# Kernel optimization log

Measured on AMD Instinct MI355X. Metric: run time of the kernel, lower is better.

Reference implementation:

```python
import jax, jax.numpy as jnp
import numpy as np
from jax import lax

B, S, T = 32, 128, 64          # batch, src_len, trg_len
E, H = 64, 512                 # embed_dim, hidden_size
SRC_V, TRG_V = 32000, 32000


def gru_cell(x, h, W_ih, W_hh, b_ih, b_hh):
    """PyTorch-convention GRU cell. x:[B,I], h:[B,H] -> h':[B,H]"""
    gi = x @ W_ih.T + b_ih            # [B,3H]
    gh = h @ W_hh.T + b_hh            # [B,3H]
    i_r, i_z, i_n = jnp.split(gi, 3, axis=-1)
    h_r, h_z, h_n = jnp.split(gh, 3, axis=-1)
    r = jax.nn.sigmoid(i_r + h_r)
    z = jax.nn.sigmoid(i_z + h_z)
    n = jnp.tanh(i_n + r * h_n)
    return (1.0 - z) * n + z * h


def setup_inputs() -> dict:
    key = jax.random.key(0)
    ks = jax.random.split(key, 22)
    g = lambda i, shape: jax.random.normal(ks[i], shape, jnp.float32) * 0.05
    return {
        "src": jax.random.randint(ks[0], (B, S), 0, SRC_V),
        "trg": jax.random.randint(ks[1], (B, T), 0, TRG_V),
        "src_embed": g(2, (SRC_V, E)),
        "trg_embed": g(3, (TRG_V, E)),
        # encoder GRU (1 layer, input E)
        "enc_W_ih": g(4, (3 * H, E)), "enc_W_hh": g(5, (3 * H, H)),
        "enc_b_ih": g(6, (3 * H,)), "enc_b_hh": g(7, (3 * H,)),
        # decoder GRU layer 0 (input E+H due to attention concat)
        "dec0_W_ih": g(8, (3 * H, E + H)), "dec0_W_hh": g(9, (3 * H, H)),
        "dec0_b_ih": g(10, (3 * H,)), "dec0_b_hh": g(11, (3 * H,)),
        # decoder GRU layer 1 (input H)
        "dec1_W_ih": g(12, (3 * H, H)), "dec1_W_hh": g(13, (3 * H, H)),
        "dec1_b_ih": g(14, (3 * H,)), "dec1_b_hh": g(15, (3 * H,)),
        # additive attention: energy = tanh(W[h;enc]) , score = v^T energy
        "attn_W": g(16, (H, 2 * H)), "attn_b": g(17, (H,)),
        "v_W": g(18, (1, H)), "v_b": jnp.zeros((1,), jnp.float32),
        # output projection H -> TRG_V
        "fc_W": g(19, (TRG_V, H)), "fc_b": jnp.zeros((TRG_V,), jnp.float32),
    }


def reference(src, trg, src_embed, trg_embed,
              enc_W_ih, enc_W_hh, enc_b_ih, enc_b_hh,
              dec0_W_ih, dec0_W_hh, dec0_b_ih, dec0_b_hh,
              dec1_W_ih, dec1_W_hh, dec1_b_ih, dec1_b_hh,
              attn_W, attn_b, v_W, v_b, fc_W, fc_b):
    batch = src.shape[0]
    src_e = src_embed[src]                              # [B,S,E]

    # ---- encoder: 1-layer GRU over src ----
    def enc_step(h, x):
        h2 = gru_cell(x, h, enc_W_ih, enc_W_hh, enc_b_ih, enc_b_hh)
        return h2, h2
    h0 = jnp.zeros((batch, H), src_e.dtype)
    h_last, enc_outs = lax.scan(enc_step, h0, jnp.swapaxes(src_e, 0, 1))
    enc_outs = jnp.swapaxes(enc_outs, 0, 1)             # [B,S,H]

    # _adapt_hidden: replicate last encoder layer to 2 decoder layers
    carry0 = (h_last, h_last)

    # ---- decoder: teacher forcing (ratio=1.0), steps t=1..T-1 ----
    def dec_step(carry, tok):
        h0_, h1_ = carry
        # attention context from top decoder layer hidden
        q = jnp.concatenate(
            [jnp.broadcast_to(h1_[:, None, :], enc_outs.shape), enc_outs], axis=-1)  # [B,S,2H]
        energy = jnp.tanh(q @ attn_W.T + attn_b)        # [B,S,H]
        scores = energy @ v_W[0] + v_b[0]               # [B,S]
        w = jax.nn.softmax(scores, axis=-1)
        context = jnp.einsum('bs,bsh->bh', w, enc_outs) # [B,H]
        emb = jnp.concatenate([trg_embed[tok], context], axis=-1)  # [B,E+H]
        h0n = gru_cell(emb, h0_, dec0_W_ih, dec0_W_hh, dec0_b_ih, dec0_b_hh)
        h1n = gru_cell(h0n, h1_, dec1_W_ih, dec1_W_hh, dec1_b_ih, dec1_b_hh)
        logits = h1n @ fc_W.T + fc_b                    # [B,V]
        return (h0n, h1n), logits

    tokens = jnp.swapaxes(trg[:, :-1], 0, 1)            # inputs for t=1..T-1
    _, logits = lax.scan(dec_step, carry0, tokens)      # [T-1,B,V]
    outputs = jnp.concatenate(
        [jnp.zeros((batch, 1, TRG_V), logits.dtype), jnp.swapaxes(logits, 0, 1)], axis=1)
    return outputs                                       # [B,T,V]
```

## Files before the change

kernel.cpp:

```cpp
#include <hip/hip_runtime.h>
#include <hip/hip_bf16.h>

#define BB 32
#define SS 128
#define TT 64
#define EE 64
#define HH 512
#define H3 1536
#define VV 32000
#define EHD 576
#define TD 63
#define MFC 2048

typedef unsigned short u16;
typedef unsigned int   u32;

typedef __attribute__((ext_vector_type(8))) short bf16x8;
typedef __attribute__((ext_vector_type(4))) float f32x4;

__device__ __forceinline__ float bf2f(u16 u){ return __uint_as_float(((u32)u)<<16); }
__device__ __forceinline__ u16 f2bf(float f){
  u32 u = __float_as_uint(f);
  u += 0x7FFFu + ((u>>16)&1u);
  return (u16)(u>>16);
}
__device__ __forceinline__ float sigm(float x){ return 1.f/(1.f+__expf(-x)); }
__device__ __forceinline__ float tanh_f(float x){ return 1.f - 2.f/(1.f+__expf(2.f*x)); }

__device__ __forceinline__ void bf8f(uint4 q, float* f){
  f[0]=__uint_as_float(q.x<<16); f[1]=__uint_as_float(q.x&0xFFFF0000u);
  f[2]=__uint_as_float(q.y<<16); f[3]=__uint_as_float(q.y&0xFFFF0000u);
  f[4]=__uint_as_float(q.z<<16); f[5]=__uint_as_float(q.z&0xFFFF0000u);
  f[6]=__uint_as_float(q.w<<16); f[7]=__uint_as_float(q.w&0xFFFF0000u);
}

template<bool BF>
__device__ __forceinline__ void wload8(const void* base, size_t eoff, float* f){
  if constexpr (BF){
    uint4 q = *(const uint4*)((const u16*)base + eoff);
    bf8f(q, f);
  } else {
    const float4* p = (const float4*)((const float*)base + eoff);
    float4 a = p[0], b = p[1];
    f[0]=a.x; f[1]=a.y; f[2]=a.z; f[3]=a.w;
    f[4]=b.x; f[5]=b.y; f[6]=b.z; f[7]=b.w;
  }
}
template<bool BF>
__device__ __forceinline__ float wld(const void* base, size_t eoff){
  if constexpr (BF) return bf2f(((const u16*)base)[eoff]);
  else              return ((const float*)base)[eoff];
}
template<bool BF>
__device__ __forceinline__ void stage32(const void* gbase, size_t eoff, u16* lds){
  if constexpr (BF){
    const uint4* g = (const uint4*)((const u16*)gbase + eoff);
    uint4* l = (uint4*)lds;
    l[0]=g[0]; l[1]=g[1]; l[2]=g[2]; l[3]=g[3];
  } else {
    const float4* g = (const float4*)((const float*)gbase + eoff);
    #pragma unroll
    for(int i=0;i<8;i++){
      float4 v = g[i];
      u16* d = lds + i*4;
      d[0]=f2bf(v.x); d[1]=f2bf(v.y); d[2]=f2bf(v.z); d[3]=f2bf(v.w);
    }
  }
}

__global__ __launch_bounds__(64) void k_detect(const void* w, int* flag){
  int tid = threadIdx.x;
  const u16* p = (const u16*)w;
  float m = 0.f;
  #pragma unroll
  for(int i=0;i<16;i++){
    float v = fabsf(bf2f(p[tid*16+i]));
    m = fmaxf(m, v);
  }
  #pragma unroll
  for(int off=32;off;off>>=1) m = fmaxf(m, __shfl_down(m, off));
  if(tid==0) *flag = (m < 16.f) ? 1 : 0;
}

template<bool BF>
__device__ void emb_gi_body(const int* toks, int tstride, const void* emb_tab,
                            const void* W_ih, int wstride, const void* b_ih,
                            float* gi)
{
  int blk = blockIdx.x;
  int jc = blk % 6; int b = (blk/6) % BB; int t = blk/(6*BB);
  int tid = threadIdx.x;
  int tok = toks[b*tstride + t];
  __shared__ float emb[EE];
  if(tid < EE) emb[tid] = wld<BF>(emb_tab, (size_t)tok*EE + tid);
  __syncthreads();
  int j = jc*256 + tid;
  float acc = wld<BF>(b_ih, j);
  size_t roff = (size_t)j*wstride;
  #pragma unroll
  for(int i=0;i<8;i++){
    float f[8]; wload8<BF>(W_ih, roff + i*8, f);
    #pragma unroll
    for(int l=0;l<8;l++) acc += emb[i*8+l]*f[l];
  }
  gi[((size_t)t*BB + b)*H3 + j] = acc;
}
__global__ __launch_bounds__(256) void k_emb_gi(
    const int* flag, const int* toks, int tstride, const void* emb_tab,
    const void* W_ih, int wstride, const void* b_ih, float* gi)
{
  if(*flag) emb_gi_body<true>(toks,tstride,emb_tab,W_ih,wstride,b_ih,gi);
  else      emb_gi_body<false>(toks,tstride,emb_tab,W_ih,wstride,b_ih,gi);
}

template<bool BF>
__device__ void enc_step_body(const float* hin, float* hout,
                              const void* W_hh, const void* b_hh,
                              const float* gi_t, float* enc_outs, int t,
                              float* h0init, float* h1init)
{
  int b = blockIdx.x >> 3, q = blockIdx.x & 7;
  int tid = threadIdx.x;
  __shared__ float hs[HH];
  __shared__ float red[3][256];
  const float* hrow = hin + b*HH;
  hs[tid] = hrow[tid]; hs[tid+256] = hrow[tid+256];
  __syncthreads();
  int jj = tid >> 2, t4 = tid & 3;
  int j = q*64 + jj;
  int k0 = t4*128;
  float ar=0.f, az=0.f, an=0.f;
  size_t orr = (size_t)j*HH + k0;
  size_t oz = (size_t)(512+j)*HH + k0;
  size_t on = (size_t)(1024+j)*HH + k0;
  #pragma unroll 4
  for(int i=0;i<16;i++){
    float f[8];
    wload8<BF>(W_hh, orr + i*8, f);
    #pragma unroll
    for(int l=0;l<8;l++) ar += hs[k0+i*8+l]*f[l];
    wload8<BF>(W_hh, oz + i*8, f);
    #pragma unroll
    for(int l=0;l<8;l++) az += hs[k0+i*8+l]*f[l];
    wload8<BF>(W_hh, on + i*8, f);
    #pragma unroll
    for(int l=0;l<8;l++) an += hs[k0+i*8+l]*f[l];
  }
  red[0][tid]=ar; red[1][tid]=az; red[2][tid]=an;
  __syncthreads();
  if(t4==0){
    float gr = red[0][tid]+red[0][tid+1]+red[0][tid+2]+red[0][tid+3] + wld<BF>(b_hh, j);
    float gz = red[1][tid]+red[1][tid+1]+red[1][tid+2]+red[1][tid+3] + wld<BF>(b_hh, 512+j);
    float gn = red[2][tid]+red[2][tid+1]+red[2][tid+2]+red[2][tid+3] + wld<BF>(b_hh, 1024+j);
    const float* gib = gi_t + b*H3;
    float r = sigm(gib[j] + gr);
    float z = sigm(gib[512+j] + gz);
    float n = tanh_f(gib[1024+j] + r*gn);
    float hn = (1.f - z)*n + z*hs[j];
    hout[b*HH + j] = hn;
    enc_outs[((size_t)b*SS + t)*HH + j] = hn;
    if(h0init){ h0init[b*HH+j] = hn; h1init[b*HH+j] = hn; }
  }
}
__global__ __launch_bounds__(256) void k_enc_step(
    const int* flag, const float* hin, float* hout,
    const void* W_hh, const void* b_hh, const float* gi_t,
    float* enc_outs, int t, float* h0init, float* h1init)
{
  if(*flag) enc_step_body<true>(hin,hout,W_hh,b_hh,gi_t,enc_outs,t,h0init,h1init);
  else      enc_step_body<false>(hin,hout,W_hh,b_hh,gi_t,enc_outs,t,h0init,h1init);
}

template<bool BF>
__device__ void attn_proj_body(const float* enc_outs, const void* attn_W,
                               const void* attn_b, float* P)
{
  int blk = blockIdx.x;
  int jc = blk & 1; int s = (blk>>1) & (SS-1); int b = blk >> 8;
  int tid = threadIdx.x;
  __shared__ float es[HH];
  const float* er = enc_outs + ((size_t)b*SS + s)*HH;
  es[tid]=er[tid]; es[tid+256]=er[tid+256];
  __syncthreads();
  int j = jc*256 + tid;
  size_t roff = (size_t)j*1024 + 512;
  float acc = wld<BF>(attn_b, j);
  #pragma unroll 4
  for(int i=0;i<64;i++){
    float f[8]; wload8<BF>(attn_W, roff + i*8, f);
    #pragma unroll
    for(int l=0;l<8;l++) acc += es[i*8+l]*f[l];
  }
  P[((size_t)b*SS+s)*HH + j] = acc;
}
__global__ __launch_bounds__(256) void k_attn_proj(
  const int* flag, const float* enc_outs, const void* attn_W,
  const void* attn_b, float* P)
{
  if(*flag) attn_proj_body<true>(enc_outs, attn_W, attn_b, P);
  else      attn_proj_body<false>(enc_outs, attn_W, attn_b, P);
}

template<bool BF>
__device__ void dec_A_body(const float* h1, const void* attn_W, float* Abuf)
{
  int b = blockIdx.x >> 1, jc = blockIdx.x & 1;
  int tid = threadIdx.x;
  __shared__ float hsr[HH];
  hsr[tid]=h1[b*HH+tid]; hsr[tid+256]=h1[b*HH+tid+256];
  __syncthreads();
  int j = jc*256 + tid;
  size_t roff = (size_t)j*1024;
  float acc = 0.f;
  #pragma unroll 4
  for(int i=0;i<64;i++){
    float f[8]; wload8<BF>(attn_W, roff + i*8, f);
    #pragma unroll
    for(int l=0;l<8;l++) acc += hsr[i*8+l]*f[l];
  }
  Abuf[b*HH + j] = acc;
}
__global__ __launch_bounds__(256) void k_dec_A(
  const int* flag, const float* h1, const void* attn_W, float* Abuf)
{
  if(*flag) dec_A_body<true>(h1, attn_W, Abuf);
  else      dec_A_body<false>(h1, attn_W, Abuf);
}

template<bool BF>
__device__ void dec_scores_body(const float* Abuf, const float* P,
                                const float* enc_outs, const void* vW,
                                const void* vb, float* Cpart, float* Ssum)
{
  int b = blockIdx.x >> 3, sb = blockIdx.x & 7;
  int tid = threadIdx.x;
  __shared__ float As[HH];
  __shared__ float vs[HH];
  __shared__ float eS[16];
  As[tid]=Abuf[b*HH+tid]; As[tid+256]=Abuf[b*HH+tid+256];
  vs[tid]=wld<BF>(vW, tid); vs[tid+256]=wld<BF>(vW, tid+256);
  __syncthreads();
  int wave = tid>>6, lane = tid&63;
  float vbf = wld<BF>(vb, 0);
  #pragma unroll
  for(int i=0;i<4;i++){
    int s = sb*16 + wave*4 + i;
    const float* Prow = P + ((size_t)b*SS+s)*HH;
    float part = 0.f;
    #pragma unroll
    for(int kk=0;kk<8;kk++){
      int k = lane + kk*64;
      part += vs[k]*tanh_f(As[k]+Prow[k]);
    }
    #pragma unroll
    for(int off=32;off;off>>=1) part += __shfl_down(part, off);
    if(lane==0) eS[wave*4+i] = __expf(part + vbf);
  }
  __syncthreads();
  for(int j=tid;j<HH;j+=256){
    float c = 0.f;
    #pragma unroll 4
    for(int i=0;i<16;i++) c += eS[i]*enc_outs[((size_t)b*SS + sb*16+i)*HH + j];
    Cpart[((size_t)b*8+sb)*HH + j] = c;
  }
  if(tid==0){ float ss=0.f; for(int i=0;i<16;i++) ss+=eS[i]; Ssum[b*8+sb]=ss; }
}
__global__ __launch_bounds__(256) void k_dec_scores(
  const int* flag, const float* Abuf, const float* P, const float* enc_outs,
  const void* vW, const void* vb, float* Cpart, float* Ssum)
{
  if(*flag) dec_scores_body<true>(Abuf,P,enc_outs,vW,vb,Cpart,Ssum);
  else      dec_scores_body<false>(Abuf,P,enc_outs,vW,vb,Cpart,Ssum);
}

template<bool BF>
__device__ void dec_h0_body(const float* h0in, float* h0out,
                            const float* Cpart, const float* Ssum,
                            const void* W_ih, const void* W_hh,
                            const void* b_hh, const float* gi_t)
{
  int b = blockIdx.x >> 3, q = blockIdx.x & 7;
  int tid = threadIdx.x;
  __shared__ float ctx[HH];
  __shared__ float hs[HH];
  __shared__ float red[6][256];
  const float* hr = h0in + b*HH;
  hs[tid]=hr[tid]; hs[tid+256]=hr[tid+256];
  float ssum = 0.f;
  #pragma unroll
  for(int sb=0;sb<8;sb++) ssum += Ssum[b*8+sb];
  float invS = 1.f/ssum;
  for(int j=tid;j<HH;j+=256){
    float c = 0.f;
    #pragma unroll
    for(int sb=0;sb<8;sb++) c += Cpart[((size_t)b*8+sb)*HH + j];
    ctx[j] = c*invS;
  }
  __syncthreads();
  int jj = tid>>2, t4 = tid&3, j = q*64+jj, k0 = t4*128;
  float pr=0.f,pz=0.f,pn=0.f,qr=0.f,qz=0.f,qn=0.f;
  size_t oir = (size_t)j*EHD + 64 + k0;
  size_t oiz = (size_t)(512+j)*EHD + 64 + k0;
  size_t oin = (size_t)(1024+j)*EHD + 64 + k0;
  size_t ohr = (size_t)j*HH + k0;
  size_t ohz = (size_t)(512+j)*HH + k0;
  size_t ohn = (size_t)(1024+j)*HH + k0;
  #pragma unroll 2
  for(int i=0;i<16;i++){
    float f[8];
    wload8<BF>(W_ih, oir + i*8, f);
    #pragma unroll
    for(int l=0;l<8;l++) pr += ctx[k0+i*8+l]*f[l];
    wload8<BF>(W_ih, oiz + i*8, f);
    #pragma unroll
    for(int l=0;l<8;l++) pz += ctx[k0+i*8+l]*f[l];
    wload8<BF>(W_ih, oin + i*8, f);
    #pragma unroll
    for(int l=0;l<8;l++) pn += ctx[k0+i*8+l]*f[l];
    wload8<BF>(W_hh, ohr + i*8, f);
    #pragma unroll
    for(int l=0;l<8;l++) qr += hs[k0+i*8+l]*f[l];
    wload8<BF>(W_hh, ohz + i*8, f);
    #pragma unroll
    for(int l=0;l<8;l++) qz += hs[k0+i*8+l]*f[l];
    wload8<BF>(W_hh, ohn + i*8, f);
    #pragma unroll
    for(int l=0;l<8;l++) qn += hs[k0+i*8+l]*f[l];
  }
  red[0][tid]=pr; red[1][tid]=pz; red[2][tid]=pn;
  red[3][tid]=qr; red[4][tid]=qz; red[5][tid]=qn;
  __syncthreads();
  if(t4==0){
    float gir = gi_t[b*H3 + j]        + red[0][tid]+red[0][tid+1]+red[0][tid+2]+red[0][tid+3];
    float giz = gi_t[b*H3 + 512 + j]  + red[1][tid]+red[1][tid+1]+red[1][tid+2]+red[1][tid+3];
    float gin = gi_t[b*H3 + 1024 + j] + red[2][tid]+red[2][tid+1]+red[2][tid+2]+red[2][tid+3];
    float ghr = red[3][tid]+red[3][tid+1]+red[3][tid+2]+red[3][tid+3] + wld<BF>(b_hh, j);
    float ghz = red[4][tid]+red[4][tid+1]+red[4][tid+2]+red[4][tid+3] + wld<BF>(b_hh, 512+j);
    float ghn = red[5][tid]+red[5][tid+1]+red[5][tid+2]+red[5][tid+3] + wld<BF>(b_hh, 1024+j);
    float r = sigm(gir+ghr), z = sigm(giz+ghz), n = tanh_f(gin + r*ghn);
    h0out[b*HH + j] = (1.f - z)*n + z*hs[j];
  }
}
__global__ __launch_bounds__(256) void k_dec_h0(
  const int* flag, const float* h0in, float* h0out,
  const float* Cpart, const float* Ssum,
  const void* W_ih, const void* W_hh, const void* b_hh, const float* gi_t)
{
  if(*flag) dec_h0_body<true>(h0in,h0out,Cpart,Ssum,W_ih,W_hh,b_hh,gi_t);
  else      dec_h0_body<false>(h0in,h0out,Cpart,Ssum,W_ih,W_hh,b_hh,gi_t);
}

template<bool BF>
__device__ void dec_h1_body(const float* xin, const float* h1in, float* h1out,
                            const void* W_ih, const void* b_ih,
                            const void* W_hh, const void* b_hh,
                            u16* h1_all_t)
{
  int b = blockIdx.x >> 3, q = blockIdx.x & 7;
  int tid = threadIdx.x;
  __shared__ float xs[HH];
  __shared__ float hs[HH];
  __shared__ float red[6][256];
  const float* xr = xin + b*HH;
  const float* hr = h1in + b*HH;
  xs[tid]=xr[tid]; xs[tid+256]=xr[tid+256];
  hs[tid]=hr[tid]; hs[tid+256]=hr[tid+256];
  __syncthreads();
  int jj = tid>>2, t4 = tid&3, j = q*64+jj, k0 = t4*128;
  float pr=0.f,pz=0.f,pn=0.f,qr=0.f,qz=0.f,qn=0.f;
  size_t oir = (size_t)j*HH + k0;
  size_t oiz = (size_t)(512+j)*HH + k0;
  size_t oin = (size_t)(1024+j)*HH + k0;
  #pragma unroll 2
  for(int i=0;i<16;i++){
    float f[8];
    wload8<BF>(W_ih, oir + i*8, f);
    #pragma unroll
    for(int l=0;l<8;l++) pr += xs[k0+i*8+l]*f[l];
    wload8<BF>(W_ih, oiz + i*8, f);
    #pragma unroll
    for(int l=0;l<8;l++) pz += xs[k0+i*8+l]*f[l];
    wload8<BF>(W_ih, oin + i*8, f);
    #pragma unroll
    for(int l=0;l<8;l++) pn += xs[k0+i*8+l]*f[l];
    wload8<BF>(W_hh, oir + i*8, f);
    #pragma unroll
    for(int l=0;l<8;l++) qr += hs[k0+i*8+l]*f[l];
    wload8<BF>(W_hh, oiz + i*8, f);
    #pragma unroll
    for(int l=0;l<8;l++) qz += hs[k0+i*8+l]*f[l];
    wload8<BF>(W_hh, oin + i*8, f);
    #pragma unroll
    for(int l=0;l<8;l++) qn += hs[k0+i*8+l]*f[l];
  }
  red[0][tid]=pr; red[1][tid]=pz; red[2][tid]=pn;
  red[3][tid]=qr; red[4][tid]=qz; red[5][tid]=qn;
  __syncthreads();
  if(t4==0){
    float gir = wld<BF>(b_ih, j)      + red[0][tid]+red[0][tid+1]+red[0][tid+2]+red[0][tid+3];
    float giz = wld<BF>(b_ih, 512+j)  + red[1][tid]+red[1][tid+1]+red[1][tid+2]+red[1][tid+3];
    float gin = wld<BF>(b_ih, 1024+j) + red[2][tid]+red[2][tid+1]+red[2][tid+2]+red[2][tid+3];
    float ghr = red[3][tid]+red[3][tid+1]+red[3][tid+2]+red[3][tid+3] + wld<BF>(b_hh, j);
    float ghz = red[4][tid]+red[4][tid+1]+red[4][tid+2]+red[4][tid+3] + wld<BF>(b_hh, 512+j);
    float ghn = red[5][tid]+red[5][tid+1]+red[5][tid+2]+red[5][tid+3] + wld<BF>(b_hh, 1024+j);
    float r = sigm(gir+ghr), z = sigm(giz+ghz), n = tanh_f(gin + r*ghn);
    float hn = (1.f - z)*n + z*hs[j];
    h1out[b*HH + j] = hn;
    h1_all_t[b*HH + j] = f2bf(hn);
  }
}
__global__ __launch_bounds__(256) void k_dec_h1(
  const int* flag, const float* xin, const float* h1in, float* h1out,
  const void* W_ih, const void* b_ih, const void* W_hh, const void* b_hh,
  u16* h1_all_t)
{
  if(*flag) dec_h1_body<true>(xin,h1in,h1out,W_ih,b_ih,W_hh,b_hh,h1_all_t);
  else      dec_h1_body<false>(xin,h1in,h1out,W_ih,b_ih,W_hh,b_hh,h1_all_t);
}

__global__ __launch_bounds__(256) void k_zero_t0(const int* flag, void* out){
  int idx = blockIdx.x*256 + threadIdx.x;
  int b = idx / VV, v = idx - b*VV;
  size_t o = (size_t)b*TT*VV + v;
  if(*flag) ((u16*)out)[o] = 0;
  else      ((float*)out)[o] = 0.f;
}

template<bool BF>
__device__ void fc_body(const u16* A, const void* W, const void* bias, void* out)
{
  __shared__ u16 As[128*72];
  __shared__ u16 Bs[128*72];
  int bm = blockIdx.x, bn = blockIdx.y;
  int tid = threadIdx.x;
  int wave = tid>>6, lane = tid&63;
  int wr = wave>>1, wc = wave&1;
  f32x4 acc[4][4];
  f32x4 zero = {0.f,0.f,0.f,0.f};
  #pragma unroll
  for(int i=0;i<4;i++)
    #pragma unroll
    for(int j=0;j<4;j++) acc[i][j]=zero;

  int row = tid>>1, half = tid&1;
  const size_t gA = (size_t)(bm*128 + row)*512 + half*32;
  const size_t gB = (size_t)(bn*128 + row)*512 + half*32;
  u16* lA = As + row*72 + half*32;
  u16* lB = Bs + row*72 + half*32;

  for(int kk=0;kk<8;kk++){
    int k0 = kk*64;
    if(kk) __syncthreads();
    stage32<true>(A, gA + k0, lA);
    stage32<BF>(W, gB + k0, lB);
    __syncthreads();
    #pragma unroll
    for(int ks=0;ks<2;ks++){
      int kof = ks*32 + (lane>>4)*8;
      bf16x8 af[4], bfv[4];
      #pragma unroll
      for(int i=0;i<4;i++){
        af[i]  = *(const bf16x8*)(As + (wr*64 + i*16 + (lane&15))*72 + kof);
        bfv[i] = *(const bf16x8*)(Bs + (wc*64 + i*16 + (lane&15))*72 + kof);
      }
      #pragma unroll
      for(int i=0;i<4;i++)
        #pragma unroll
        for(int j=0;j<4;j++)
          acc[i][j] = __builtin_amdgcn_mfma_f32_16x16x32_bf16(af[i], bfv[j], acc[i][j], 0, 0, 0);
    }
  }
  int quad = lane>>4, col = lane&15;
  #pragma unroll
  for(int j=0;j<4;j++){
    int n = bn*128 + wc*64 + j*16 + col;
    float bsv = wld<BF>(bias, n);
    #pragma unroll
    for(int i=0;i<4;i++){
      int mbase = bm*128 + wr*64 + i*16 + quad*4;
      #pragma unroll
      for(int r=0;r<4;r++){
        int m = mbase + r;
        if(m < TD*BB){
          int t = m >> 5, b = m & 31;
          size_t o = ((size_t)(b*TT + t + 1))*VV + n;
          float v = acc[i][j][r] + bsv;
          if constexpr (BF) ((u16*)out)[o] = f2bf(v);
          else              ((float*)out)[o] = v;
        }
      }
    }
  }
}
__global__ __launch_bounds__(256) void k_fc(
  const int* flag, const u16* A, const void* W, const void* bias, void* out)
{
  if(*flag) fc_body<true>(A, W, bias, out);
  else      fc_body<false>(A, W, bias, out);
}

extern "C" void kernel_launch(void* const* d_in, const int* in_sizes, int n_in,
                              void* d_out, int out_size, void* d_ws, size_t ws_size,
                              hipStream_t stream)
{
  const int* src = (const int*)d_in[0];
  const int* trg = (const int*)d_in[1];
  const void* src_emb = d_in[2];
  const void* trg_emb = d_in[3];
  const void* eWih = d_in[4];
  const void* eWhh = d_in[5];
  const void* ebih = d_in[6];
  const void* ebhh = d_in[7];
  const void* d0Wih = d_in[8];
  const void* d0Whh = d_in[9];
  const void* d0bih = d_in[10];
  const void* d0bhh = d_in[11];
  const void* d1Wih = d_in[12];
  const void* d1Whh = d_in[13];
  const void* d1bih = d_in[14];
  const void* d1bhh = d_in[15];
  const void* aW  = d_in[16];
  const void* ab  = d_in[17];
  const void* vW  = d_in[18];
  const void* vb  = d_in[19];
  const void* fcW = d_in[20];
  const void* fcb = d_in[21];

  char* w = (char*)d_ws;
  int*   flag    = (int*)w;   w += 16;
  float* enc_gi  = (float*)w; w += (size_t)SS*BB*H3*4;
  float* trg_gi  = (float*)w; w += (size_t)TD*BB*H3*4;
  float* enc_outs= (float*)w; w += (size_t)BB*SS*HH*4;
  float* P       = (float*)w; w += (size_t)BB*SS*HH*4;
  float* hE      = (float*)w; w += (size_t)2*BB*HH*4;
  float* h0b     = (float*)w; w += (size_t)2*BB*HH*4;
  float* h1b     = (float*)w; w += (size_t)2*BB*HH*4;
  float* Abuf    = (float*)w; w += (size_t)BB*HH*4;
  float* Cpart   = (float*)w; w += (size_t)BB*8*HH*4;
  float* Ssum    = (float*)w; w += (size_t)BB*8*4;
  u16*   h1_all  = (u16*)w;   w += (size_t)MFC*HH*2;

  hipMemsetAsync(hE, 0, BB*HH*4, stream);
  hipMemsetAsync(h1_all + (size_t)TD*BB*HH, 0, 32*HH*2, stream);

  k_detect<<<1,64,0,stream>>>(fcW, flag);

  k_emb_gi<<<SS*BB*6, 256, 0, stream>>>(flag, src, SS, src_emb, eWih, EE, ebih, enc_gi);
  k_emb_gi<<<TD*BB*6, 256, 0, stream>>>(flag, trg, TT, trg_emb, d0Wih, EHD, d0bih, trg_gi);

  for(int t=0;t<SS;t++){
    k_enc_step<<<256,256,0,stream>>>(
      flag, hE + (t&1)*BB*HH, hE + ((t+1)&1)*BB*HH,
      eWhh, ebhh, enc_gi + (size_t)t*BB*H3, enc_outs, t,
      (t==SS-1)?h0b:(float*)nullptr, (t==SS-1)?h1b:(float*)nullptr);
  }

  k_attn_proj<<<BB*SS*2,256,0,stream>>>(flag, enc_outs, aW, ab, P);

  for(int t=0;t<TD;t++){
    int pi = t&1, po = (t+1)&1;
    k_dec_A<<<64,256,0,stream>>>(flag, h1b + pi*BB*HH, aW, Abuf);
    k_dec_scores<<<256,256,0,stream>>>(flag, Abuf, P, enc_outs, vW, vb, Cpart, Ssum);
    k_dec_h0<<<256,256,0,stream>>>(flag, h0b+pi*BB*HH, h0b+po*BB*HH, Cpart, Ssum,
                                   d0Wih, d0Whh, d0bhh, trg_gi + (size_t)t*BB*H3);
    k_dec_h1<<<256,256,0,stream>>>(flag, h0b+po*BB*HH, h1b+pi*BB*HH, h1b+po*BB*HH,
                                   d1Wih, d1bih, d1Whh, d1bhh, h1_all + (size_t)t*BB*HH);
  }

  k_zero_t0<<<(BB*VV)/256, 256, 0, stream>>>(flag, d_out);
  dim3 g(16, 250);
  k_fc<<<g, 256, 0, stream>>>(flag, h1_all, fcW, fcb, d_out);
}
```

Before: 7.828 ms.

## Fuse encoder/decoder recurrence into one persistent cooperative kernel with grid syncs

Replaces the hundreds of per-timestep kernel launches (encoder steps, attention projection, and four decoder stages per step) with a single cooperative kernel of 256 blocks that loops over time and uses grid-wide syncs between stages. Shared memory is unified into one struct reused across stages, and dec_A is re-partitioned to split the K dimension across 4 threads per output so it fits the 256-block layout. This removes launch overhead and inter-kernel gaps on the serial recurrence. In exchange, every stage pays for a grid barrier, and the attention projection becomes a serial loop of 32 iterations per block.

```diff
diff --git a/kernel.cpp b/kernel.cpp
--- a/kernel.cpp
+++ b/kernel.cpp
@@ -1,5 +1,8 @@
 #include <hip/hip_runtime.h>
 #include <hip/hip_bf16.h>
+#include <hip/hip_cooperative_groups.h>
+
+namespace cg = cooperative_groups;
 
 #define BB 32
 #define SS 128
@@ -113,16 +116,40 @@
   else      emb_gi_body<false>(toks,tstride,emb_tab,W_ih,wstride,b_ih,gi);
 }
 
-template<bool BF>
-__device__ void enc_step_body(const float* hin, float* hout,
-                              const void* W_hh, const void* b_hh,
-                              const float* gi_t, float* enc_outs, int t,
-                              float* h0init, float* h1init)
-{
-  int b = blockIdx.x >> 3, q = blockIdx.x & 7;
-  int tid = threadIdx.x;
-  __shared__ float hs[HH];
-  __shared__ float red[3][256];
+struct SMem {
+  float a[HH];
+  float b[HH];
+  float red[6][256];
+  float eS[16];
+};
+
+struct EncDecParams {
+  const int* flag;
+  const void *eWhh, *ebhh;
+  const float* enc_gi;
+  float* enc_outs;
+  const void *aW, *ab, *vW, *vb;
+  const void *d0Wih, *d0Whh, *d0bhh;
+  const float* trg_gi;
+  const void *d1Wih, *d1bih, *d1Whh, *d1bhh;
+  float* hE;
+  float* h0b;
+  float* h1b;
+  float* P;
+  float* Abuf;
+  float* Cpart;
+  float* Ssum;
+  u16* h1_all;
+};
+
+template<bool BF>
+__device__ void enc_step_dev(SMem& sm, int b, int q, int tid,
+                             const float* hin, float* hout,
+                             const void* W_hh, const void* b_hh,
+                             const float* gi_t, float* enc_outs, int t,
+                             float* h0init, float* h1init)
+{
+  float* hs = sm.b;
   const float* hrow = hin + b*HH;
   hs[tid] = hrow[tid]; hs[tid+256] = hrow[tid+256];
   __syncthreads();
@@ -146,12 +173,12 @@
     #pragma unroll
     for(int l=0;l<8;l++) an += hs[k0+i*8+l]*f[l];
   }
-  red[0][tid]=ar; red[1][tid]=az; red[2][tid]=an;
+  sm.red[0][tid]=ar; sm.red[1][tid]=az; sm.red[2][tid]=an;
   __syncthreads();
   if(t4==0){
-    float gr = red[0][tid]+red[0][tid+1]+red[0][tid+2]+red[0][tid+3] + wld<BF>(b_hh, j);
-    float gz = red[1][tid]+red[1][tid+1]+red[1][tid+2]+red[1][tid+3] + wld<BF>(b_hh, 512+j);
-    float gn = red[2][tid]+red[2][tid+1]+red[2][tid+2]+red[2][tid+3] + wld<BF>(b_hh, 1024+j);
+    float gr = sm.red[0][tid]+sm.red[0][tid+1]+sm.red[0][tid+2]+sm.red[0][tid+3] + wld<BF>(b_hh, j);
+    float gz = sm.red[1][tid]+sm.red[1][tid+1]+sm.red[1][tid+2]+sm.red[1][tid+3] + wld<BF>(b_hh, 512+j);
+    float gn = sm.red[2][tid]+sm.red[2][tid+1]+sm.red[2][tid+2]+sm.red[2][tid+3] + wld<BF>(b_hh, 1024+j);
     const float* gib = gi_t + b*H3;
     float r = sigm(gib[j] + gr);
     float z = sigm(gib[512+j] + gz);
@@ -162,23 +189,14 @@
     if(h0init){ h0init[b*HH+j] = hn; h1init[b*HH+j] = hn; }
   }
 }
-__global__ __launch_bounds__(256) void k_enc_step(
-    const int* flag, const float* hin, float* hout,
-    const void* W_hh, const void* b_hh, const float* gi_t,
-    float* enc_outs, int t, float* h0init, float* h1init)
-{
-  if(*flag) enc_step_body<true>(hin,hout,W_hh,b_hh,gi_t,enc_outs,t,h0init,h1init);
-  else      enc_step_body<false>(hin,hout,W_hh,b_hh,gi_t,enc_outs,t,h0init,h1init);
-}
-
-template<bool BF>
-__device__ void attn_proj_body(const float* enc_outs, const void* attn_W,
-                               const void* attn_b, float* P)
-{
-  int blk = blockIdx.x;
-  int jc = blk & 1; int s = (blk>>1) & (SS-1); int b = blk >> 8;
-  int tid = threadIdx.x;
-  __shared__ float es[HH];
+
+template<bool BF>
+__device__ void attn_proj_dev(SMem& sm, int tid, int item,
+                              const float* enc_outs, const void* attn_W,
+                              const void* attn_b, float* P)
+{
+  int jc = item & 1; int s = (item>>1) & (SS-1); int b = item >> 8;
+  float* es = sm.a;
   const float* er = enc_outs + ((size_t)b*SS + s)*HH;
   es[tid]=er[tid]; es[tid+256]=er[tid+256];
   __syncthreads();
@@ -192,51 +210,40 @@
     for(int l=0;l<8;l++) acc += es[i*8+l]*f[l];
   }
   P[((size_t)b*SS+s)*HH + j] = acc;
-}
-__global__ __launch_bounds__(256) void k_attn_proj(
-  const int* flag, const float* enc_outs, const void* attn_W,
-  const void* attn_b, float* P)
-{
-  if(*flag) attn_proj_body<true>(enc_outs, attn_W, attn_b, P);
-  else      attn_proj_body<false>(enc_outs, attn_W, attn_b, P);
-}
-
-template<bool BF>
-__device__ void dec_A_body(const float* h1, const void* attn_W, float* Abuf)
-{
-  int b = blockIdx.x >> 1, jc = blockIdx.x & 1;
-  int tid = threadIdx.x;
-  __shared__ float hsr[HH];
+  __syncthreads();
+}
+
+template<bool BF>
+__device__ void dec_A_dev(SMem& sm, int b, int q, int tid,
+                          const float* h1, const void* attn_W, float* Abuf)
+{
+  float* hsr = sm.b;
   hsr[tid]=h1[b*HH+tid]; hsr[tid+256]=h1[b*HH+tid+256];
   __syncthreads();
-  int j = jc*256 + tid;
-  size_t roff = (size_t)j*1024;
+  int jj = tid>>2, t4 = tid&3, j = q*64+jj, k0 = t4*128;
+  size_t roff = (size_t)j*1024 + k0;
   float acc = 0.f;
   #pragma unroll 4
-  for(int i=0;i<64;i++){
+  for(int i=0;i<16;i++){
     float f[8]; wload8<BF>(attn_W, roff + i*8, f);
     #pragma unroll
-    for(int l=0;l<8;l++) acc += hsr[i*8+l]*f[l];
-  }
-  Abuf[b*HH + j] = acc;
-}
-__global__ __launch_bounds__(256) void k_dec_A(
-  const int* flag, const float* h1, const void* attn_W, float* Abuf)
-{
-  if(*flag) dec_A_body<true>(h1, attn_W, Abuf);
-  else      dec_A_body<false>(h1, attn_W, Abuf);
-}
-
-template<bool BF>
-__device__ void dec_scores_body(const float* Abuf, const float* P,
-                                const float* enc_outs, const void* vW,
-                                const void* vb, float* Cpart, float* Ssum)
-{
-  int b = blockIdx.x >> 3, sb = blockIdx.x & 7;
-  int tid = threadIdx.x;
-  __shared__ float As[HH];
-  __shared__ float vs[HH];
-  __shared__ float eS[16];
+    for(int l=0;l<8;l++) acc += hsr[k0+i*8+l]*f[l];
+  }
+  sm.red[0][tid]=acc;
+  __syncthreads();
+  if(t4==0){
+    Abuf[b*HH + j] = sm.red[0][tid]+sm.red[0][tid+1]+sm.red[0][tid+2]+sm.red[0][tid+3];
+  }
+}
+
+template<bool BF>
+__device__ void dec_scores_dev(SMem& sm, int b, int sb, int tid,
+                               const float* Abuf, const float* P,
+                               const float* enc_outs, const void* vW,
+                               const void* vb, float* Cpart, float* Ssum)
+{
+  float* As = sm.a;
+  float* vs = sm.b;
   As[tid]=Abuf[b*HH+tid]; As[tid+256]=Abuf[b*HH+tid+256];
   vs[tid]=wld<BF>(vW, tid); vs[tid+256]=wld<BF>(vW, tid+256);
   __syncthreads();
@@ -254,36 +261,27 @@
     }
     #pragma unroll
     for(int off=32;off;off>>=1) part += __shfl_down(part, off);
-    if(lane==0) eS[wave*4+i] = __expf(part + vbf);
+    if(lane==0) sm.eS[wave*4+i] = __expf(part + vbf);
   }
   __syncthreads();
   for(int j=tid;j<HH;j+=256){
     float c = 0.f;
     #pragma unroll 4
-    for(int i=0;i<16;i++) c += eS[i]*enc_outs[((size_t)b*SS + sb*16+i)*HH + j];
+    for(int i=0;i<16;i++) c += sm.eS[i]*enc_outs[((size_t)b*SS + sb*16+i)*HH + j];
     Cpart[((size_t)b*8+sb)*HH + j] = c;
   }
-  if(tid==0){ float ss=0.f; for(int i=0;i<16;i++) ss+=eS[i]; Ssum[b*8+sb]=ss; }
-}
-__global__ __launch_bounds__(256) void k_dec_scores(
-  const int* flag, const float* Abuf, const float* P, const float* enc_outs,
-  const void* vW, const void* vb, float* Cpart, float* Ssum)
-{
-  if(*flag) dec_scores_body<true>(Abuf,P,enc_outs,vW,vb,Cpart,Ssum);
-  else      dec_scores_body<false>(Abuf,P,enc_outs,vW,vb,Cpart,Ssum);
-}
-
-template<bool BF>
-__device__ void dec_h0_body(const float* h0in, float* h0out,
-                            const float* Cpart, const float* Ssum,
-                            const void* W_ih, const void* W_hh,
-                            const void* b_hh, const float* gi_t)
-{
-  int b = blockIdx.x >> 3, q = blockIdx.x & 7;
-  int tid = threadIdx.x;
-  __shared__ float ctx[HH];
-  __shared__ float hs[HH];
-  __shared__ float red[6][256];
+  if(tid==0){ float ss=0.f; for(int i=0;i<16;i++) ss+=sm.eS[i]; Ssum[b*8+sb]=ss; }
+}
+
+template<bool BF>
+__device__ void dec_h0_dev(SMem& sm, int b, int q, int tid,
+                           const float* h0in, float* h0out,
+                           const float* Cpart, const float* Ssum,
+                           const void* W_ih, const void* W_hh,
+                           const void* b_hh, const float* gi_t)
+{
+  float* ctx = sm.a;
+  float* hs  = sm.b;
   const float* hr = h0in + b*HH;
   hs[tid]=hr[tid]; hs[tid+256]=hr[tid+256];
   float ssum = 0.f;
@@ -327,40 +325,30 @@
     #pragma unroll
     for(int l=0;l<8;l++) qn += hs[k0+i*8+l]*f[l];
   }
-  red[0][tid]=pr; red[1][tid]=pz; red[2][tid]=pn;
-  red[3][tid]=qr; red[4][tid]=qz; red[5][tid]=qn;
+  sm.red[0][tid]=pr; sm.red[1][tid]=pz; sm.red[2][tid]=pn;
+  sm.red[3][tid]=qr; sm.red[4][tid]=qz; sm.red[5][tid]=qn;
   __syncthreads();
   if(t4==0){
-    float gir = gi_t[b*H3 + j]        + red[0][tid]+red[0][tid+1]+red[0][tid+2]+red[0][tid+3];
-    float giz = gi_t[b*H3 + 512 + j]  + red[1][tid]+red[1][tid+1]+red[1][tid+2]+red[1][tid+3];
-    float gin = gi_t[b*H3 + 1024 + j] + red[2][tid]+red[2][tid+1]+red[2][tid+2]+red[2][tid+3];
-    float ghr = red[3][tid]+red[3][tid+1]+red[3][tid+2]+red[3][tid+3] + wld<BF>(b_hh, j);
-    float ghz = red[4][tid]+red[4][tid+1]+red[4][tid+2]+red[4][tid+3] + wld<BF>(b_hh, 512+j);
-    float ghn = red[5][tid]+red[5][tid+1]+red[5][tid+2]+red[5][tid+3] + wld<BF>(b_hh, 1024+j);
+    float gir = gi_t[b*H3 + j]        + sm.red[0][tid]+sm.red[0][tid+1]+sm.red[0][tid+2]+sm.red[0][tid+3];
+    float giz = gi_t[b*H3 + 512 + j]  + sm.red[1][tid]+sm.red[1][tid+1]+sm.red[1][tid+2]+sm.red[1][tid+3];
+    float gin = gi_t[b*H3 + 1024 + j] + sm.red[2][tid]+sm.red[2][tid+1]+sm.red[2][tid+2]+sm.red[2][tid+3];
+    float ghr = sm.red[3][tid]+sm.red[3][tid+1]+sm.red[3][tid+2]+sm.red[3][tid+3] + wld<BF>(b_hh, j);
+    float ghz = sm.red[4][tid]+sm.red[4][tid+1]+sm.red[4][tid+2]+sm.red[4][tid+3] + wld<BF>(b_hh, 512+j);
+    float ghn = sm.red[5][tid]+sm.red[5][tid+1]+sm.red[5][tid+2]+sm.red[5][tid+3] + wld<BF>(b_hh, 1024+j);
     float r = sigm(gir+ghr), z = sigm(giz+ghz), n = tanh_f(gin + r*ghn);
     h0out[b*HH + j] = (1.f - z)*n + z*hs[j];
   }
 }
-__global__ __launch_bounds__(256) void k_dec_h0(
-  const int* flag, const float* h0in, float* h0out,
-  const float* Cpart, const float* Ssum,
-  const void* W_ih, const void* W_hh, const void* b_hh, const float* gi_t)
-{
-  if(*flag) dec_h0_body<true>(h0in,h0out,Cpart,Ssum,W_ih,W_hh,b_hh,gi_t);
-  else      dec_h0_body<false>(h0in,h0out,Cpart,Ssum,W_ih,W_hh,b_hh,gi_t);
-}
-
-template<bool BF>
-__device__ void dec_h1_body(const float* xin, const float* h1in, float* h1out,
-                            const void* W_ih, const void* b_ih,
-                            const void* W_hh, const void* b_hh,
-                            u16* h1_all_t)
-{
-  int b = blockIdx.x >> 3, q = blockIdx.x & 7;
-  int tid = threadIdx.x;
-  __shared__ float xs[HH];
-  __shared__ float hs[HH];
-  __shared__ float red[6][256];
+
+template<bool BF>
+__device__ void dec_h1_dev(SMem& sm, int b, int q, int tid,
+                           const float* xin, const float* h1in, float* h1out,
+                           const void* W_ih, const void* b_ih,
+                           const void* W_hh, const void* b_hh,
+                           u16* h1_all_t)
+{
+  float* xs = sm.a;
+  float* hs = sm.b;
   const float* xr = xin + b*HH;
   const float* hr = h1in + b*HH;
   xs[tid]=xr[tid]; xs[tid+256]=xr[tid+256];
@@ -393,29 +381,67 @@
     #pragma unroll
     for(int l=0;l<8;l++) qn += hs[k0+i*8+l]*f[l];
   }
-  red[0][tid]=pr; red[1][tid]=pz; red[2][tid]=pn;
-  red[3][tid]=qr; red[4][tid]=qz; red[5][tid]=qn;
+  sm.red[0][tid]=pr; sm.red[1][tid]=pz; sm.red[2][tid]=pn;
+  sm.red[3][tid]=qr; sm.red[4][tid]=qz; sm.red[5][tid]=qn;
   __syncthreads();
   if(t4==0){
-    float gir = wld<BF>(b_ih, j)      + red[0][tid]+red[0][tid+1]+red[0][tid+2]+red[0][tid+3];
-    float giz = wld<BF>(b_ih, 512+j)  + red[1][tid]+red[1][tid+1]+red[1][tid+2]+red[1][tid+3];
-    float gin = wld<BF>(b_ih, 1024+j) + red[2][tid]+red[2][tid+1]+red[2][tid+2]+red[2][tid+3];
-    float ghr = red[3][tid]+red[3][tid+1]+red[3][tid+2]+red[3][tid+3] + wld<BF>(b_hh, j);
-    float ghz = red[4][tid]+red[4][tid+1]+red[4][tid+2]+red[4][tid+3] + wld<BF>(b_hh, 512+j);
-    float ghn = red[5][tid]+red[5][tid+1]+red[5][tid+2]+red[5][tid+3] + wld<BF>(b_hh, 1024+j);
+    float gir = wld<BF>(b_ih, j)      + sm.red[0][tid]+sm.red[0][tid+1]+sm.red[0][tid+2]+sm.red[0][tid+3];
+    float giz = wld<BF>(b_ih, 512+j)  + sm.red[1][tid]+sm.red[1][tid+1]+sm.red[1][tid+2]+sm.red[1][tid+3];
+    float gin = wld<BF>(b_ih, 1024+j) + sm.red[2][tid]+sm.red[2][tid+1]+sm.red[2][tid+2]+sm.red[2][tid+3];
+    float ghr = sm.red[3][tid]+sm.red[3][tid+1]+sm.red[3][tid+2]+sm.red[3][tid+3] + wld<BF>(b_hh, j);
+    float ghz = sm.red[4][tid]+sm.red[4][tid+1]+sm.red[4][tid+2]+sm.red[4][tid+3] + wld<BF>(b_hh, 512+j);
+    float ghn = sm.red[5][tid]+sm.red[5][tid+1]+sm.red[5][tid+2]+sm.red[5][tid+3] + wld<BF>(b_hh, 1024+j);
     float r = sigm(gir+ghr), z = sigm(giz+ghz), n = tanh_f(gin + r*ghn);
     float hn = (1.f - z)*n + z*hs[j];
     h1out[b*HH + j] = hn;
     h1_all_t[b*HH + j] = f2bf(hn);
   }
 }
-__global__ __launch_bounds__(256) void k_dec_h1(
-  const int* flag, const float* xin, const float* h1in, float* h1out,
-  const void* W_ih, const void* b_ih, const void* W_hh, const void* b_hh,
-  u16* h1_all_t)
-{
-  if(*flag) dec_h1_body<true>(xin,h1in,h1out,W_ih,b_ih,W_hh,b_hh,h1_all_t);
-  else      dec_h1_body<false>(xin,h1in,h1out,W_ih,b_ih,W_hh,b_hh,h1_all_t);
+
+template<bool BF>
+__device__ void encdec_body(const EncDecParams& p, cg::grid_group& g, SMem& sm)
+{
+  int blk = blockIdx.x, tid = threadIdx.x;
+  int b = blk >> 3, q = blk & 7;
+
+  for(int t=0;t<SS;t++){
+    enc_step_dev<BF>(sm, b, q, tid,
+        p.hE + (t&1)*BB*HH, p.hE + ((t+1)&1)*BB*HH,
+        p.eWhh, p.ebhh, p.enc_gi + (size_t)t*BB*H3, p.enc_outs, t,
+        (t==SS-1)? p.h0b : (float*)nullptr,
+        (t==SS-1)? p.h1b : (float*)nullptr);
+    g.sync();
+  }
+
+  for(int it=0; it<(BB*SS*2)/256; it++){
+    attn_proj_dev<BF>(sm, tid, it*256 + blk, p.enc_outs, p.aW, p.ab, p.P);
+  }
+  g.sync();
+
+  for(int t=0;t<TD;t++){
+    int pi = t&1, po = (t+1)&1;
+    dec_A_dev<BF>(sm, b, q, tid, p.h1b + pi*BB*HH, p.aW, p.Abuf);
+    g.sync();
+    dec_scores_dev<BF>(sm, b, q, tid, p.Abuf, p.P, p.enc_outs, p.vW, p.vb,
+                       p.Cpart, p.Ssum);
+    g.sync();
+    dec_h0_dev<BF>(sm, b, q, tid, p.h0b + pi*BB*HH, p.h0b + po*BB*HH,
+                   p.Cpart, p.Ssum, p.d0Wih, p.d0Whh, p.d0bhh,
+                   p.trg_gi + (size_t)t*BB*H3);
+    g.sync();
+    dec_h1_dev<BF>(sm, b, q, tid, p.h0b + po*BB*HH, p.h1b + pi*BB*HH,
+                   p.h1b + po*BB*HH, p.d1Wih, p.d1bih, p.d1Whh, p.d1bhh,
+                   p.h1_all + (size_t)t*BB*HH);
+    g.sync();
+  }
+}
+
+__global__ __launch_bounds__(256) void k_encdec(EncDecParams p)
+{
+  cg::grid_group g = cg::this_grid();
+  __shared__ SMem sm;
+  if(*p.flag) encdec_body<true>(p, g, sm);
+  else        encdec_body<false>(p, g, sm);
 }
 
 __global__ __launch_bounds__(256) void k_zero_t0(const int* flag, void* out){
@@ -548,24 +574,22 @@
   k_emb_gi<<<SS*BB*6, 256, 0, stream>>>(flag, src, SS, src_emb, eWih, EE, ebih, enc_gi);
   k_emb_gi<<<TD*BB*6, 256, 0, stream>>>(flag, trg, TT, trg_emb, d0Wih, EHD, d0bih, trg_gi);
 
-  for(int t=0;t<SS;t++){
-    k_enc_step<<<256,256,0,stream>>>(
-      flag, hE + (t&1)*BB*HH, hE + ((t+1)&1)*BB*HH,
-      eWhh, ebhh, enc_gi + (size_t)t*BB*H3, enc_outs, t,
-      (t==SS-1)?h0b:(float*)nullptr, (t==SS-1)?h1b:(float*)nullptr);
-  }
-
-  k_attn_proj<<<BB*SS*2,256,0,stream>>>(flag, enc_outs, aW, ab, P);
-
-  for(int t=0;t<TD;t++){
-    int pi = t&1, po = (t+1)&1;
-    k_dec_A<<<64,256,0,stream>>>(flag, h1b + pi*BB*HH, aW, Abuf);
-    k_dec_scores<<<256,256,0,stream>>>(flag, Abuf, P, enc_outs, vW, vb, Cpart, Ssum);
-    k_dec_h0<<<256,256,0,stream>>>(flag, h0b+pi*BB*HH, h0b+po*BB*HH, Cpart, Ssum,
-                                   d0Wih, d0Whh, d0bhh, trg_gi + (size_t)t*BB*H3);
-    k_dec_h1<<<256,256,0,stream>>>(flag, h0b+po*BB*HH, h1b+pi*BB*HH, h1b+po*BB*HH,
-                                   d1Wih, d1bih, d1Whh, d1bhh, h1_all + (size_t)t*BB*HH);
-  }
+  EncDecParams prm;
+  prm.flag = flag;
+  prm.eWhh = eWhh; prm.ebhh = ebhh;
+  prm.enc_gi = enc_gi;
+  prm.enc_outs = enc_outs;
+  prm.aW = aW; prm.ab = ab; prm.vW = vW; prm.vb = vb;
+  prm.d0Wih = d0Wih; prm.d0Whh = d0Whh; prm.d0bhh = d0bhh;
+  prm.trg_gi = trg_gi;
+  prm.d1Wih = d1Wih; prm.d1bih = d1bih; prm.d1Whh = d1Whh; prm.d1bhh = d1bhh;
+  prm.hE = hE; prm.h0b = h0b; prm.h1b = h1b;
+  prm.P = P; prm.Abuf = Abuf; prm.Cpart = Cpart; prm.Ssum = Ssum;
+  prm.h1_all = h1_all;
+
+  void* kargs[] = { (void*)&prm };
+  hipLaunchCooperativeKernel(reinterpret_cast<void*>(&k_encdec),
+                             dim3(256), dim3(256), kargs, 0, stream);
 
   k_zero_t0<<<(BB*VV)/256, 256, 0, stream>>>(flag, d_out);
   dim3 g(16, 250);
```

Measured after the change: 17.61 ms. 2.25x slower.
